# Performance work log

Hardware: AMD Instinct MI355X
Metric: run time of the kernel (lower is better)

## Reference

```python
import jax, jax.numpy as jnp
import numpy as np

GROUP_SIZE = 128

def setup_inputs() -> dict:
    key = jax.random.key(0)
    k0, k1, k2, k3 = jax.random.split(key, 4)
    B, S, K, N = 4, 16, 8192, 28672
    G = GROUP_SIZE
    x = jax.random.normal(k0, (B, S, K), dtype=jnp.float16)
    # packed uint8 stored as int32 (2 int4 nibbles per byte along K)
    w_packed = jax.random.randint(k1, (K // 2, N), 0, 256, dtype=jnp.int32)
    # per-group positive scales, typical magnitude for int4 quant of fp16 weights
    scales = (jax.random.uniform(k2, (K // G, N), dtype=jnp.float32) * 0.02 + 1e-4).astype(jnp.float16)
    bias = (jax.random.normal(k3, (N,), dtype=jnp.float16) * 0.02).astype(jnp.float16)
    return {"x": x, "w_packed": w_packed, "scales": scales, "bias": bias}

def _dequant(w_packed, scales):
    # w_packed: [K//2, N] ints in [0,256); low nibble -> even k, high nibble -> odd k
    low = (w_packed & 15) - 8          # [K//2, N] int32 in [-8, 7]
    high = ((w_packed >> 4) & 15) - 8  # [K//2, N]
    Kh, N = w_packed.shape
    w_int = jnp.stack([low, high], axis=1).reshape(Kh * 2, N)  # interleave -> [K, N]
    s = jnp.repeat(scales, GROUP_SIZE, axis=0)                 # [K, N] fp16
    return w_int.astype(jnp.float16) * s                       # [K, N] fp16

def reference(x, w_packed, scales, bias):
    # x: [B, S, K] fp16 -> y: [B, S, N] fp16
    w = _dequant(w_packed, scales)                 # [K, N] fp16
    lead = x.shape[:-1]
    x2 = x.reshape(-1, x.shape[-1])                # [M, K]
    # fp32 accumulation, fp16 output (matches Triton kernel's tl.dot accumulator)
    y = jnp.dot(x2, w, preferred_element_type=jnp.float32).astype(jnp.float16)
    y = y + bias
    return y.reshape(*lead, -1)
```

## Files before the change

kernel.cpp:

```cpp
#include <hip/hip_runtime.h>


typedef short  short8  __attribute__((ext_vector_type(8)));
typedef float  float4v __attribute__((ext_vector_type(4)));
typedef int    int4v   __attribute__((ext_vector_type(4)));
typedef unsigned int uint4v __attribute__((ext_vector_type(4)));

constexpr int Kd = 8192;
constexpr int Nd = 28672;
constexpr int KSPLIT = 4;

__device__ __forceinline__ unsigned f32_to_bf16_rn(float f) {
    unsigned u = __builtin_bit_cast(unsigned, f);
    return (u + 0x7FFFu + ((u >> 16) & 1u)) >> 16;
}

__device__ __forceinline__ void async16(const void* g, void* l) {
    __builtin_amdgcn_global_load_lds(
        (const __attribute__((address_space(1))) unsigned*)g,
        (__attribute__((address_space(3))) unsigned*)l, 16, 0, 0);
}

__global__ __launch_bounds__(256)
void init_y_kernel(const float* __restrict__ bias, float* __restrict__ y) {
    const int gid = blockIdx.x * 256 + threadIdx.x;
    const int m  = gid / (Nd / 4);
    const int nq = gid % (Nd / 4);
    ((float4v*)y)[(long)m * (Nd / 4) + nq] = ((const float4v*)bias)[nq];
}

__global__ __launch_bounds__(256)
void cvt_x_kernel(const float* __restrict__ x, unsigned short* __restrict__ o) {
    const int i = (blockIdx.x * 256 + threadIdx.x) * 8;
    float4v a = *(const float4v*)(x + i);
    float4v b = *(const float4v*)(x + i + 4);
    union { unsigned short s[8]; short8 v; } r;
    #pragma unroll
    for (int j = 0; j < 4; ++j) {
        r.s[j]     = (unsigned short)f32_to_bf16_rn(a[j]);
        r.s[4 + j] = (unsigned short)f32_to_bf16_rn(b[j]);
    }
    *(short8*)(o + i) = r.v;
}

__global__ __launch_bounds__(256, 4)
void int4_main_kernel(const unsigned short* __restrict__ xw,
                      const int*            __restrict__ wp,
                      const float*          __restrict__ scales,
                      float*                __restrict__ y)
{
    __shared__ unsigned wb0[2048], wb1[2048];
    __shared__ unsigned xb0[2048], xb1[2048];
    __shared__ unsigned sb[1024];

    const int t = threadIdx.x, lane = t & 63, wv = t >> 6;
    const int q = lane >> 4, c = lane & 15;
    const int l4 = lane >> 4, l15 = lane & 15;
    const int n0 = blockIdx.x * 64, kz = blockIdx.y;

    const int* wsrc0; const int* wsrc1;
    {
        int r0 = wv * 8 + 0 * 4 + l4, c0 = (l15 * 4) ^ (((wv * 2 + 0) & 3) << 4);
        int r1 = wv * 8 + 1 * 4 + l4, c1 = (l15 * 4) ^ (((wv * 2 + 1) & 3) << 4);
        wsrc0 = wp + (long)(kz * 1024 + r0) * Nd + n0 + c0;
        wsrc1 = wp + (long)(kz * 1024 + r1) * Nd + n0 + c1;
    }
    const unsigned short* xsrc0; const unsigned short* xsrc1;
    {
        int s0 = wv * 128 + 0 * 64 + lane, m0 = s0 >> 3, k0 = (s0 & 7) ^ (m0 & 7);
        int s1 = wv * 128 + 1 * 64 + lane, m1 = s1 >> 3, k1 = (s1 & 7) ^ (m1 & 7);
        xsrc0 = xw + (long)m0 * Kd + kz * 2048 + k0 * 8;
        xsrc1 = xw + (long)m1 * Kd + kz * 2048 + k1 * 8;
    }
    const int ldof = wv * 512;

    {
        const float* ssrc = scales + (long)(kz * 16 + (t >> 4)) * Nd + n0 + (t & 15) * 4;
        async16(ssrc, sb + wv * 256);
    }
    async16(wsrc0, wb0 + ldof);
    async16(wsrc1, wb0 + ldof + 256);
    async16(xsrc0, xb0 + ldof);
    async16(xsrc1, xb0 + ldof + 256);

    float4v acc[4] = {};

    auto stage = [&](int hg, unsigned* wbuf, unsigned* xbuf) {
        const long wof = (long)hg * 32 * Nd;
        const long xof = (long)hg * 64;
        async16(wsrc0 + wof, wbuf + ldof);
        async16(wsrc1 + wof, wbuf + ldof + 256);
        async16(xsrc0 + xof, xbuf + ldof);
        async16(xsrc1 + xof, xbuf + ldof + 256);
    };

    auto compute = [&](const unsigned* wbuf, const unsigned* xbuf, int g) {
        const float s   = __builtin_bit_cast(float, sb[g * 64 + wv * 16 + c]);
        const float m8s = -8.0f * s;
        #pragma unroll
        for (int it = 0; it < 2; ++it) {
            union { short8 h; unsigned u[4]; } bu;
            #pragma unroll
            for (int i = 0; i < 4; ++i) {
                unsigned v = wbuf[(it * 16 + q * 4 + i) * 64 + ((wv * 16 + c) ^ (q << 4))];
                float lo = fmaf((float)(v & 15u), s, m8s);
                float hi = fmaf((float)((v >> 4) & 15u), s, m8s);
                bu.u[i] = f32_to_bf16_rn(lo) | (f32_to_bf16_rn(hi) << 16);
            }
            #pragma unroll
            for (int mt = 0; mt < 4; ++mt) {
                int m = mt * 16 + c;
                int slot = m * 8 + ((it * 4 + q) ^ (c & 7));
                short8 a = *(const short8*)(xbuf + slot * 4);
                acc[mt] = __builtin_amdgcn_mfma_f32_16x16x32_bf16(a, bu.h, acc[mt], 0, 0, 0);
            }
        }
    };

    for (int hgp = 0; hgp < 16; ++hgp) {
        const int hg = 2 * hgp;
        stage(hg + 1, wb1, xb1);
        asm volatile("s_waitcnt vmcnt(4)\ns_barrier" ::: "memory");
        compute(wb0, xb0, hgp);
        asm volatile("s_waitcnt lgkmcnt(0)\ns_barrier" ::: "memory");
        if (hgp < 15) {
            stage(hg + 2, wb0, xb0);
            asm volatile("s_waitcnt vmcnt(4)\ns_barrier" ::: "memory");
        } else {
            asm volatile("s_waitcnt vmcnt(0)\ns_barrier" ::: "memory");
        }
        compute(wb1, xb1, hgp);
        asm volatile("s_waitcnt lgkmcnt(0)\ns_barrier" ::: "memory");
    }

    const int nw = n0 + wv * 16 + c;
    #pragma unroll
    for (int mt = 0; mt < 4; ++mt)
        #pragma unroll
        for (int r = 0; r < 4; ++r)
            atomicAdd(&y[(long)(mt * 16 + q * 4 + r) * Nd + nw], acc[mt][r]);
}

__global__ __launch_bounds__(256, 6)
void int4_main_nows_kernel(const float* __restrict__ xf,
                           const int*   __restrict__ wp,
                           const float* __restrict__ scales,
                           float*       __restrict__ y)
{
    constexpr int LDS_STRIDE = 68;
    __shared__ unsigned lds_w[64 * LDS_STRIDE];
    const int t = threadIdx.x, lane = t & 63, wv = t >> 6;
    const int q = lane >> 4, c = lane & 15;
    const int n0 = blockIdx.x * 64, kz = blockIdx.y;
    const int sr = t >> 4, ss = t & 15;
    const int*   wp_b = wp + (long)(kz * 1024 + sr) * Nd + n0 + 4 * ss;
    const float* sc_b = scales + (long)(kz * 16) * Nd + n0 + 4 * ss;
    const float* xf_b = xf + (long)c * Kd + kz * 2048 + q * 8;
    float4v acc[4] = {};

    for (int g = 0; g < 16; ++g) {
        const float4v s4 = *(const float4v*)(sc_b + (long)g * Nd);
        const int* wg = wp_b + (long)g * 64 * Nd;
        #pragma unroll
        for (int i = 0; i < 4; ++i) {
            int4v v = *(const int4v*)(wg + (long)i * 16 * Nd);
            uint4v pk;
            #pragma unroll
            for (int j = 0; j < 4; ++j) {
                float lo = (float)((v[j] & 15) - 8) * s4[j];
                float hi = (float)(((v[j] >> 4) & 15) - 8) * s4[j];
                pk[j] = f32_to_bf16_rn(lo) | (f32_to_bf16_rn(hi) << 16);
            }
            *(uint4v*)&lds_w[(i * 16 + sr) * LDS_STRIDE + 4 * ss] = pk;
        }
        __syncthreads();
        const float* xg = xf_b + g * 128;
        #pragma unroll
        for (int it = 0; it < 4; ++it) {
            union { short8 h; unsigned u[4]; } bu;
            #pragma unroll
            for (int i = 0; i < 4; ++i)
                bu.u[i] = lds_w[(it * 16 + q * 4 + i) * LDS_STRIDE + wv * 16 + c];
            const short8 b = bu.h;
            const float* xk = xg + it * 32;
            #pragma unroll
            for (int mt = 0; mt < 4; ++mt) {
                float4v a0 = *(const float4v*)(xk + (long)mt * 16 * Kd);
                float4v a1 = *(const float4v*)(xk + (long)mt * 16 * Kd + 4);
                union { unsigned short s[8]; short8 v; } r;
                #pragma unroll
                for (int j = 0; j < 4; ++j) {
                    r.s[j]     = (unsigned short)f32_to_bf16_rn(a0[j]);
                    r.s[4 + j] = (unsigned short)f32_to_bf16_rn(a1[j]);
                }
                acc[mt] = __builtin_amdgcn_mfma_f32_16x16x32_bf16(r.v, b, acc[mt], 0, 0, 0);
            }
        }
        __syncthreads();
    }
    const int nw = n0 + wv * 16 + c;
    #pragma unroll
    for (int mt = 0; mt < 4; ++mt)
        #pragma unroll
        for (int r = 0; r < 4; ++r)
            atomicAdd(&y[(long)(mt * 16 + q * 4 + r) * Nd + nw], acc[mt][r]);
}

extern "C" void kernel_launch(void* const* d_in, const int* in_sizes, int n_in,
                              void* d_out, int out_size, void* d_ws, size_t ws_size,
                              hipStream_t stream) {
    const float* x      = (const float*)d_in[0];
    const int*   wp     = (const int*)d_in[1];
    const float* scales = (const float*)d_in[2];
    const float* bias   = (const float*)d_in[3];
    float*       y      = (float*)d_out;

    init_y_kernel<<<dim3(1792), dim3(256), 0, stream>>>(bias, y);

    const size_t xb_bytes = (size_t)64 * Kd * sizeof(unsigned short);
    dim3 grid(Nd / 64, KSPLIT);
    dim3 block(256);

    if (ws_size >= xb_bytes) {
        unsigned short* xb = (unsigned short*)d_ws;
        cvt_x_kernel<<<dim3(256), dim3(256), 0, stream>>>(x, xb);
        int4_main_kernel<<<grid, block, 0, stream>>>(xb, wp, scales, y);
    } else {
        int4_main_nows_kernel<<<grid, block, 0, stream>>>(x, wp, scales, y);
    }
}
```

Before: 630.7 us.

## Pre-compact packed int4 weights into swizzled byte layout before main GEMM

Adds a pre-pass kernel that squeezes the int32-stored packed weights down to one byte each. It writes them into a per-block, per-group contiguous layout with an XOR swizzle. A new main kernel then streams this compact buffer through LDS with smaller weight tiles and higher occupancy (launch bounds 5). The goal is to make the main loop's weight loads dense and coalesced instead of reading four-byte words that each carry only one useful byte. The cost is an extra full pass over the original weights plus a write and re-read of the compact copy on every call, and the path needs a larger workspace.

```diff
diff --git a/kernel.cpp b/kernel.cpp
--- a/kernel.cpp
+++ b/kernel.cpp
@@ -9,6 +9,7 @@
 constexpr int Kd = 8192;
 constexpr int Nd = 28672;
 constexpr int KSPLIT = 4;
+constexpr int NBLK = Nd / 64;
 
 __device__ __forceinline__ unsigned f32_to_bf16_rn(float f) {
     unsigned u = __builtin_bit_cast(unsigned, f);
@@ -41,6 +42,118 @@
         r.s[4 + j] = (unsigned short)f32_to_bf16_rn(b[j]);
     }
     *(short8*)(o + i) = r.v;
+}
+
+__global__ __launch_bounds__(256)
+void compact_w_kernel(const int* __restrict__ wp, unsigned* __restrict__ cw) {
+    const int b = blockIdx.x, kz = blockIdx.y, z = blockIdx.z;
+    const int t = threadIdx.x;
+    const int hg = 2 * z + (t >> 7);
+    const int u = t & 127, quad = u >> 4, cc = u & 15;
+    const int kpair0 = kz * 1024 + hg * 32 + quad * 4;
+    const int* src = wp + (long)kpair0 * Nd + b * 64 + 4 * cc;
+    int4v r0 = *(const int4v*)(src);
+    int4v r1 = *(const int4v*)(src + Nd);
+    int4v r2 = *(const int4v*)(src + 2 * Nd);
+    int4v r3 = *(const int4v*)(src + 3 * Nd);
+    uint4v o;
+    #pragma unroll
+    for (int d = 0; d < 4; ++d)
+        o[d] = (unsigned)(r0[d] & 0xFF) | ((unsigned)(r1[d] & 0xFF) << 8)
+             | ((unsigned)(r2[d] & 0xFF) << 16) | ((unsigned)(r3[d] & 0xFF) << 24);
+    unsigned* dst = cw + (long)((kz * NBLK + b) * 32 + hg) * 512
+                       + quad * 64 + ((4 * cc) ^ ((quad & 3) << 4));
+    *(uint4v*)dst = o;
+}
+
+__global__ __launch_bounds__(256, 5)
+void int4_main_cw_kernel(const unsigned short* __restrict__ xw,
+                         const unsigned*       __restrict__ cw,
+                         const float*          __restrict__ scales,
+                         float*                __restrict__ y)
+{
+    __shared__ unsigned wb0[512],  wb1[512];
+    __shared__ unsigned xb0[2048], xb1[2048];
+    __shared__ unsigned sb[1024];
+
+    const int t = threadIdx.x, lane = t & 63, wv = t >> 6;
+    const int q = lane >> 4, c = lane & 15;
+    const int n0 = blockIdx.x * 64, kz = blockIdx.y;
+
+    const unsigned* wsrc = cw + (long)((kz * NBLK + blockIdx.x) * 32) * 512
+                              + wv * 128 + lane * 4;
+    const unsigned short* xsrc0; const unsigned short* xsrc1;
+    {
+        int s0 = wv * 128 + 0 * 64 + lane, m0 = s0 >> 3, k0 = (s0 & 7) ^ (m0 & 7);
+        int s1 = wv * 128 + 1 * 64 + lane, m1 = s1 >> 3, k1 = (s1 & 7) ^ (m1 & 7);
+        xsrc0 = xw + (long)m0 * Kd + kz * 2048 + k0 * 8;
+        xsrc1 = xw + (long)m1 * Kd + kz * 2048 + k1 * 8;
+    }
+    const int ldof = wv * 512;
+
+    {
+        const float* ssrc = scales + (long)(kz * 16 + (t >> 4)) * Nd + n0 + (t & 15) * 4;
+        async16(ssrc, sb + wv * 256);
+    }
+    if (lane < 32) async16(wsrc, wb0 + wv * 128);
+    async16(xsrc0, xb0 + ldof);
+    async16(xsrc1, xb0 + ldof + 256);
+
+    float4v acc[4] = {};
+
+    auto stage = [&](int hg, unsigned* wbuf, unsigned* xbuf) {
+        const long xof = (long)hg * 64;
+        if (lane < 32) async16(wsrc + (long)hg * 512, wbuf + wv * 128);
+        async16(xsrc0 + xof, xbuf + ldof);
+        async16(xsrc1 + xof, xbuf + ldof + 256);
+    };
+
+    auto compute = [&](const unsigned* wbuf, const unsigned* xbuf, int g) {
+        const float s   = __builtin_bit_cast(float, sb[g * 64 + wv * 16 + c]);
+        const float m8s = -8.0f * s;
+        #pragma unroll
+        for (int it = 0; it < 2; ++it) {
+            unsigned v = wbuf[(it * 4 + q) * 64 + ((wv * 16 + c) ^ (q << 4))];
+            union { short8 h; unsigned u[4]; } bu;
+            #pragma unroll
+            for (int j = 0; j < 4; ++j) {
+                unsigned b = (v >> (8 * j)) & 0xFFu;
+                float lo = fmaf((float)(b & 15u), s, m8s);
+                float hi = fmaf((float)((b >> 4) & 15u), s, m8s);
+                bu.u[j] = f32_to_bf16_rn(lo) | (f32_to_bf16_rn(hi) << 16);
+            }
+            #pragma unroll
+            for (int mt = 0; mt < 4; ++mt) {
+                int m = mt * 16 + c;
+                int slot = m * 8 + ((it * 4 + q) ^ (c & 7));
+                short8 a = *(const short8*)(xbuf + slot * 4);
+                acc[mt] = __builtin_amdgcn_mfma_f32_16x16x32_bf16(a, bu.h, acc[mt], 0, 0, 0);
+            }
+        }
+    };
+
+    for (int hgp = 0; hgp < 16; ++hgp) {
+        const int hg = 2 * hgp;
+        stage(hg + 1, wb1, xb1);
+        asm volatile("s_waitcnt vmcnt(3)\ns_barrier" ::: "memory");
+        compute(wb0, xb0, hgp);
+        asm volatile("s_waitcnt lgkmcnt(0)\ns_barrier" ::: "memory");
+        if (hgp < 15) {
+            stage(hg + 2, wb0, xb0);
+            asm volatile("s_waitcnt vmcnt(3)\ns_barrier" ::: "memory");
+        } else {
+            asm volatile("s_waitcnt vmcnt(0)\ns_barrier" ::: "memory");
+        }
+        compute(wb1, xb1, hgp);
+        asm volatile("s_waitcnt lgkmcnt(0)\ns_barrier" ::: "memory");
+    }
+
+    const int nw = n0 + wv * 16 + c;
+    #pragma unroll
+    for (int mt = 0; mt < 4; ++mt)
+        #pragma unroll
+        for (int r = 0; r < 4; ++r)
+            atomicAdd(&y[(long)(mt * 16 + q * 4 + r) * Nd + nw], acc[mt][r]);
 }
 
 __global__ __launch_bounds__(256, 4)
@@ -218,10 +331,17 @@
     init_y_kernel<<<dim3(1792), dim3(256), 0, stream>>>(bias, y);
 
     const size_t xb_bytes = (size_t)64 * Kd * sizeof(unsigned short);
-    dim3 grid(Nd / 64, KSPLIT);
+    const size_t cw_bytes = (size_t)(Kd / 2) * Nd;
+    dim3 grid(NBLK, KSPLIT);
     dim3 block(256);
 
-    if (ws_size >= xb_bytes) {
+    if (ws_size >= xb_bytes + cw_bytes) {
+        unsigned short* xb = (unsigned short*)d_ws;
+        unsigned* cw = (unsigned*)((char*)d_ws + xb_bytes);
+        cvt_x_kernel<<<dim3(256), dim3(256), 0, stream>>>(x, xb);
+        compact_w_kernel<<<dim3(NBLK, KSPLIT, 16), dim3(256), 0, stream>>>(wp, cw);
+        int4_main_cw_kernel<<<grid, block, 0, stream>>>(xb, cw, scales, y);
+    } else if (ws_size >= xb_bytes) {
         unsigned short* xb = (unsigned short*)d_ws;
         cvt_x_kernel<<<dim3(256), dim3(256), 0, stream>>>(x, xb);
         int4_main_kernel<<<grid, block, 0, stream>>>(xb, wp, scales, y);
```

Measured after the change: 689.5 us. 1.09x slower.

## Triple-buffer weight and activation LDS stages and raise MFMA issue priority

Applied to the files above, without the earlier changes.

Replaces the double-buffered LDS pipeline with a three-stage ring, so two half-group loads are in flight while a third is being computed, with wait counts adjusted to match. It also wraps the MFMA sequence in s_setprio so matrix instructions win issue arbitration over other waves. The goal is to hide more global-memory latency on a bandwidth-bound int4 GEMV-like workload. In exchange LDS per block grows and launch bounds drop from 4 to 3 blocks per CU, lowering occupancy.

```diff
diff --git a/kernel.cpp b/kernel.cpp
--- a/kernel.cpp
+++ b/kernel.cpp
@@ -43,14 +43,14 @@
     *(short8*)(o + i) = r.v;
 }
 
-__global__ __launch_bounds__(256, 4)
+__global__ __launch_bounds__(256, 3)
 void int4_main_kernel(const unsigned short* __restrict__ xw,
                       const int*            __restrict__ wp,
                       const float*          __restrict__ scales,
                       float*                __restrict__ y)
 {
-    __shared__ unsigned wb0[2048], wb1[2048];
-    __shared__ unsigned xb0[2048], xb1[2048];
+    __shared__ unsigned wbA[2048], wbB[2048], wbC[2048];
+    __shared__ unsigned xbA[2048], xbB[2048], xbC[2048];
     __shared__ unsigned sb[1024];
 
     const int t = threadIdx.x, lane = t & 63, wv = t >> 6;
@@ -73,17 +73,6 @@
         xsrc1 = xw + (long)m1 * Kd + kz * 2048 + k1 * 8;
     }
     const int ldof = wv * 512;
-
-    {
-        const float* ssrc = scales + (long)(kz * 16 + (t >> 4)) * Nd + n0 + (t & 15) * 4;
-        async16(ssrc, sb + wv * 256);
-    }
-    async16(wsrc0, wb0 + ldof);
-    async16(wsrc1, wb0 + ldof + 256);
-    async16(xsrc0, xb0 + ldof);
-    async16(xsrc1, xb0 + ldof + 256);
-
-    float4v acc[4] = {};
 
     auto stage = [&](int hg, unsigned* wbuf, unsigned* xbuf) {
         const long wof = (long)hg * 32 * Nd;
@@ -94,6 +83,15 @@
         async16(xsrc1 + xof, xbuf + ldof + 256);
     };
 
+    {
+        const float* ssrc = scales + (long)(kz * 16 + (t >> 4)) * Nd + n0 + (t & 15) * 4;
+        async16(ssrc, sb + wv * 256);
+    }
+    stage(0, wbA, xbA);
+    stage(1, wbB, xbB);
+
+    float4v acc[4] = {};
+
     auto compute = [&](const unsigned* wbuf, const unsigned* xbuf, int g) {
         const float s   = __builtin_bit_cast(float, sb[g * 64 + wv * 16 + c]);
         const float m8s = -8.0f * s;
@@ -107,6 +105,7 @@
                 float hi = fmaf((float)((v >> 4) & 15u), s, m8s);
                 bu.u[i] = f32_to_bf16_rn(lo) | (f32_to_bf16_rn(hi) << 16);
             }
+            __builtin_amdgcn_s_setprio(1);
             #pragma unroll
             for (int mt = 0; mt < 4; ++mt) {
                 int m = mt * 16 + c;
@@ -114,24 +113,30 @@
                 short8 a = *(const short8*)(xbuf + slot * 4);
                 acc[mt] = __builtin_amdgcn_mfma_f32_16x16x32_bf16(a, bu.h, acc[mt], 0, 0, 0);
             }
+            __builtin_amdgcn_s_setprio(0);
         }
     };
 
-    for (int hgp = 0; hgp < 16; ++hgp) {
-        const int hg = 2 * hgp;
-        stage(hg + 1, wb1, xb1);
-        asm volatile("s_waitcnt vmcnt(4)\ns_barrier" ::: "memory");
-        compute(wb0, xb0, hgp);
+    for (int g3 = 0; g3 < 10; ++g3) {
+        const int ph = 3 * g3;
+        stage(ph + 2, wbC, xbC);
+        asm volatile("s_waitcnt vmcnt(8)\ns_barrier" ::: "memory");
+        compute(wbA, xbA, ph >> 1);
         asm volatile("s_waitcnt lgkmcnt(0)\ns_barrier" ::: "memory");
-        if (hgp < 15) {
-            stage(hg + 2, wb0, xb0);
-            asm volatile("s_waitcnt vmcnt(4)\ns_barrier" ::: "memory");
-        } else {
-            asm volatile("s_waitcnt vmcnt(0)\ns_barrier" ::: "memory");
-        }
-        compute(wb1, xb1, hgp);
+        stage(ph + 3, wbA, xbA);
+        asm volatile("s_waitcnt vmcnt(8)\ns_barrier" ::: "memory");
+        compute(wbB, xbB, (ph + 1) >> 1);
         asm volatile("s_waitcnt lgkmcnt(0)\ns_barrier" ::: "memory");
-    }
+        stage(ph + 4, wbB, xbB);
+        asm volatile("s_waitcnt vmcnt(8)\ns_barrier" ::: "memory");
+        compute(wbC, xbC, (ph + 2) >> 1);
+        asm volatile("s_waitcnt lgkmcnt(0)\ns_barrier" ::: "memory");
+    }
+    asm volatile("s_waitcnt vmcnt(4)\ns_barrier" ::: "memory");
+    compute(wbA, xbA, 15);
+    asm volatile("s_waitcnt lgkmcnt(0)\ns_barrier" ::: "memory");
+    asm volatile("s_waitcnt vmcnt(0)\ns_barrier" ::: "memory");
+    compute(wbB, xbB, 15);
 
     const int nw = n0 + wv * 16 + c;
     #pragma unroll
```

Result: no change. 627.2 us (-0.6%).
